# Kernel tuning notes

Measured on AMD Instinct MI355X. Metric: run time of the kernel, lower is better.

## Reference

```python
import jax, jax.numpy as jnp
import numpy as np
from jax import lax

B, Hm, Wm = 8, 128, 128          # batch, mesh height, mesh width
DIM, HEADS, DH, G, K = 128, 8, 64, 64, 3
INNER = HEADS * DH
N = Hm * Wm


def setup_inputs() -> dict:
    key = jax.random.key(0)
    ks = jax.random.split(key, 12)
    s = 0.02
    x = jax.random.normal(ks[0], (B, N, DIM), dtype=jnp.float32)
    conv_fx_w = jax.random.normal(ks[1], (K, K, DIM, INNER), dtype=jnp.float32) * s
    conv_fx_b = jnp.zeros((INNER,), dtype=jnp.float32)
    conv_x_w = jax.random.normal(ks[2], (K, K, DIM, INNER), dtype=jnp.float32) * s
    conv_x_b = jnp.zeros((INNER,), dtype=jnp.float32)
    # nn.Linear(dim_head, slice_num): weight (G, DH), orthogonal-init approximated by scaled normal
    slice_w = jax.random.normal(ks[3], (G, DH), dtype=jnp.float32) * (1.0 / np.sqrt(DH))
    slice_b = jnp.zeros((G,), dtype=jnp.float32)
    temperature = jnp.ones((1, HEADS, 1, 1), dtype=jnp.float32) * 0.5
    wq = jax.random.normal(ks[4], (DH, DH), dtype=jnp.float32) * s
    wk = jax.random.normal(ks[5], (DH, DH), dtype=jnp.float32) * s
    wv = jax.random.normal(ks[6], (DH, DH), dtype=jnp.float32) * s
    out_w = jax.random.normal(ks[7], (DIM, INNER), dtype=jnp.float32) * s
    out_b = jnp.zeros((DIM,), dtype=jnp.float32)
    return {
        "x": x,
        "conv_fx_w": conv_fx_w, "conv_fx_b": conv_fx_b,
        "conv_x_w": conv_x_w, "conv_x_b": conv_x_b,
        "slice_w": slice_w, "slice_b": slice_b,
        "temperature": temperature,
        "wq": wq, "wk": wk, "wv": wv,
        "out_w": out_w, "out_b": out_b,
    }


def _conv(z, w, b):
    # z: (B, H, W, Cin); w: (K, K, Cin, Cout); SAME padding, stride 1
    return lax.conv_general_dilated(
        z, w, window_strides=(1, 1), padding="SAME",
        dimension_numbers=("NHWC", "HWIO", "NHWC")) + b


def reference(x, conv_fx_w, conv_fx_b, conv_x_w, conv_x_b,
              slice_w, slice_b, temperature, wq, wk, wv, out_w, out_b):
    b, n, c = x.shape
    xi = x.reshape(b, Hm, Wm, c)
    # (B,H,W,INNER) -> (B,N,heads,dh) -> (B,heads,N,dh)
    fx_mid = _conv(xi, conv_fx_w, conv_fx_b).reshape(b, n, HEADS, DH).transpose(0, 2, 1, 3)
    x_mid = _conv(xi, conv_x_w, conv_x_b).reshape(b, n, HEADS, DH).transpose(0, 2, 1, 3)

    temp = jnp.clip(temperature, 0.1, 5.0)  # (1,heads,1,1)
    logits = (jnp.einsum("bhnc,gc->bhng", x_mid, slice_w) + slice_b) / temp
    slice_weights = jax.nn.softmax(logits, axis=-1)         # (B,heads,N,G)

    slice_norm = slice_weights.sum(axis=2)                   # (B,heads,G)
    slice_token = jnp.einsum("bhnc,bhng->bhgc", fx_mid, slice_weights)
    slice_token = slice_token / (slice_norm + 1e-5)[..., None]

    q = jnp.einsum("bhgc,dc->bhgd", slice_token, wq)
    k = jnp.einsum("bhgc,dc->bhgd", slice_token, wk)
    v = jnp.einsum("bhgc,dc->bhgd", slice_token, wv)

    scale = DH ** (-0.5)
    attn = jax.nn.softmax(jnp.einsum("bhgd,bhkd->bhgk", q, k) * scale, axis=-1)
    out_slice = jnp.einsum("bhgk,bhkd->bhgd", attn, v)       # (B,heads,G,dh)

    out_x = jnp.einsum("bhgc,bhng->bhnc", out_slice, slice_weights)
    out_x = out_x.transpose(0, 2, 1, 3).reshape(b, n, INNER)
    return jnp.einsum("bnc,dc->bnd", out_x, out_w) + out_b
```

## Files before the change

kernel.cpp:

```cpp
#include <hip/hip_runtime.h>
#include <stdint.h>

#define BATCH 8
#define HEADS 8
#define HM 128
#define WM 128
#define NPIX (HM*WM)
#define DIMC 128
#define DH 64
#define GS 64
#define INNER 512
#define KTOT 1152
#define XT_LD 128

typedef unsigned short u16;
typedef short v8s __attribute__((ext_vector_type(8)));
typedef float v4f __attribute__((ext_vector_type(4)));

__device__ __forceinline__ u16 f2bf(float f) {
    unsigned x = __float_as_uint(f);
    return (u16)((x + 0x7fffu + ((x >> 16) & 1u)) >> 16);
}
__device__ __forceinline__ float bf2f(u16 u) { return __uint_as_float(((unsigned)u) << 16); }
__device__ __forceinline__ unsigned cvtpk(float lo, float hi) {
    unsigned r;
    asm("v_cvt_pk_bf16_f32 %0, %1, %2" : "=v"(r) : "v"(lo), "v"(hi));
    return r;
}

union BF8 { uint4 v; u16 s[8]; };

__global__ __launch_bounds__(256) void k_build_w(
    const float* __restrict__ wx, const float* __restrict__ wfx,
    const float* __restrict__ slw, const float* __restrict__ temp,
    u16* __restrict__ wcatT, u16* __restrict__ wfxT)
{
    __shared__ float sw_l[GS][DH + 1];
    __shared__ float wx_l[INNER];
    int row = blockIdx.x;
    int t = threadIdx.x;
    for (int i = t; i < GS * DH; i += 256) sw_l[i >> 6][i & 63] = slw[i];
    for (int i = t; i < INNER; i += 256) wx_l[i] = wx[(size_t)row * INNER + i];
    __syncthreads();
#pragma unroll
    for (int j = 0; j < 2; j++) {
        int co = j * 256 + t;
        int h = co >> 6, g = co & 63;
        float s = 0.f;
        for (int c = 0; c < DH; c++) s = fmaf(wx_l[h * 64 + c], sw_l[g][c], s);
        float tv = fminf(fmaxf(temp[h], 0.1f), 5.0f);
        wcatT[(size_t)co * KTOT + row] = f2bf(s / tv);
        wfxT[(size_t)co * KTOT + row] = f2bf(wfx[(size_t)row * INNER + co]);
    }
}

__global__ __launch_bounds__(512) void k_build_b(
    const float* __restrict__ bx, const float* __restrict__ slw,
    const float* __restrict__ slb, const float* __restrict__ temp,
    float* __restrict__ bcatL)
{
    int co = threadIdx.x;
    int h = co >> 6, g = co & 63;
    float s = slb[g];
    for (int c = 0; c < DH; c++) s = fmaf(bx[h * 64 + c], slw[g * 64 + c], s);
    float tv = fminf(fmaxf(temp[h], 0.1f), 5.0f);
    bcatL[co] = s / tv;
}

union SmemC {
    u16 X[130 * XT_LD];
    struct { u16 SwT[64][128]; u16 FxT[64][128]; } e;
};

__global__ __launch_bounds__(256, 3) void k_conv2(
    const float* __restrict__ xin, const u16* __restrict__ wcatT,
    const u16* __restrict__ wfxT, const float* __restrict__ bcatL,
    const float* __restrict__ bfx, u16* __restrict__ swbT,
    float* __restrict__ straw, float* __restrict__ norm)
{
    __shared__ SmemC sm;
    int bid = blockIdx.x;
    int swz = (bid & 7) * 1024 + (bid >> 3);
    int b = swz >> 10;
    int r = swz & 1023;
    int y = r >> 3, h = r & 7;
    int cob = h << 6;
    int t = threadIdx.x;
    int lane = t & 63, wave = t >> 6;
    int half = wave >> 1, w_conv = wave & 1;
    int l16 = lane & 15, lk = lane >> 4;
    int bh = b * HEADS + h;

    v4f acc[4][4];
#pragma unroll
    for (int i = 0; i < 4; i++)
#pragma unroll
        for (int j = 0; j < 4; j++) acc[i][j] = v4f{0.f, 0.f, 0.f, 0.f};

    const u16* wT = w_conv ? wfxT : wcatT;
    const u16* wrb[4];
#pragma unroll
    for (int nj = 0; nj < 4; nj++)
        wrb[nj] = wT + (size_t)(cob + nj * 16 + l16) * KTOT + lk * 8;

    v8s bB[2][4];
#pragma unroll
    for (int nj = 0; nj < 4; nj++) bB[0][nj] = *(const v8s*)(wrb[nj]);

#pragma unroll
    for (int ky = 0; ky < 3; ky++) {
        int yy = y + ky - 1;
        bool yok = (unsigned)yy < (unsigned)HM;
        const float* xrow = xin + ((size_t)b * NPIX + (size_t)yy * WM) * DIMC;
        if (ky) __syncthreads();
#pragma unroll
        for (int it = 0; it < 9; it++) {
            int i = t + it * 256;
            if (i < 2080) {
                int row = i >> 4, k8 = i & 15;
                int px = row - 1;
                uint4 o;
                if (yok && (unsigned)px < (unsigned)WM) {
                    const float4* p = (const float4*)(xrow + (size_t)px * DIMC + k8 * 8);
                    float4 fa = p[0], fb = p[1];
                    o = make_uint4(cvtpk(fa.x, fa.y), cvtpk(fa.z, fa.w),
                                   cvtpk(fb.x, fb.y), cvtpk(fb.z, fb.w));
                } else {
                    o = make_uint4(0u, 0u, 0u, 0u);
                }
                *(uint4*)(sm.X + row * XT_LD + ((k8 ^ (row & 7)) * 8)) = o;
            }
        }
        __syncthreads();
#pragma unroll
        for (int cc = 0; cc < 12; cc++) {
            int gidx = ky * 12 + cc;
            if (gidx < 35) {
#pragma unroll
                for (int nj = 0; nj < 4; nj++)
                    bB[(gidx + 1) & 1][nj] = *(const v8s*)(wrb[nj] + (gidx + 1) * 32);
            }
            int kx = cc >> 2, c4 = cc & 3;
            int xr7 = (l16 + kx) & 7;
            const u16* xb = sm.X + (half * 64 + l16 + kx) * XT_LD;
            int xo = (((c4 * 4 + lk) ^ xr7) * 8);
            v8s av[4];
#pragma unroll
            for (int mi = 0; mi < 4; mi++)
                av[mi] = *(const v8s*)(xb + mi * 16 * XT_LD + xo);
#pragma unroll
            for (int mi = 0; mi < 4; mi++)
#pragma unroll
                for (int nj = 0; nj < 4; nj++)
                    acc[mi][nj] = __builtin_amdgcn_mfma_f32_16x16x32_bf16(
                        av[mi], bB[gidx & 1][nj], acc[mi][nj], 0, 0, 0);
        }
    }
    __syncthreads();

    float bb[4];
#pragma unroll
    for (int nj = 0; nj < 4; nj++)
        bb[nj] = (w_conv ? bfx : bcatL)[cob + nj * 16 + l16];

    if (w_conv == 0) {
#pragma unroll
        for (int mi = 0; mi < 4; mi++) {
#pragma unroll
            for (int q = 0; q < 4; q++) {
                float m = acc[mi][0][q] + bb[0];
#pragma unroll
                for (int nj = 1; nj < 4; nj++) m = fmaxf(m, acc[mi][nj][q] + bb[nj]);
                m = fmaxf(m, __shfl_xor(m, 1));
                m = fmaxf(m, __shfl_xor(m, 2));
                m = fmaxf(m, __shfl_xor(m, 4));
                m = fmaxf(m, __shfl_xor(m, 8));
                float ssum = 0.f;
#pragma unroll
                for (int nj = 0; nj < 4; nj++) {
                    float e = __expf(acc[mi][nj][q] + bb[nj] - m);
                    acc[mi][nj][q] = e; ssum += e;
                }
                ssum += __shfl_xor(ssum, 1);
                ssum += __shfl_xor(ssum, 2);
                ssum += __shfl_xor(ssum, 4);
                ssum += __shfl_xor(ssum, 8);
                float inv = 1.f / ssum;
#pragma unroll
                for (int nj = 0; nj < 4; nj++) acc[mi][nj][q] *= inv;
            }
        }
#pragma unroll
        for (int nj = 0; nj < 4; nj++) {
            float pn = 0.f;
#pragma unroll
            for (int mi = 0; mi < 4; mi++)
#pragma unroll
                for (int q = 0; q < 4; q++) pn += acc[mi][nj][q];
            pn += __shfl_xor(pn, 16);
            pn += __shfl_xor(pn, 32);
            if (lk == 0)
                atomicAdd(&norm[(size_t)bh * GS + nj * 16 + l16], pn);
        }
    }

#pragma unroll
    for (int nj = 0; nj < 4; nj++) {
        int grow = nj * 16 + l16;
        int r7 = l16 & 7;
#pragma unroll
        for (int mi = 0; mi < 4; mi++) {
            int p8 = half * 8 + mi * 2 + (lk >> 1);
            int off = ((p8 ^ r7) * 8) + (lk & 1) * 4;
            uint2 wv;
            if (w_conv == 0) {
                wv.x = cvtpk(acc[mi][nj][0], acc[mi][nj][1]);
                wv.y = cvtpk(acc[mi][nj][2], acc[mi][nj][3]);
                *(uint2*)&sm.e.SwT[grow][off] = wv;
            } else {
                wv.x = cvtpk(acc[mi][nj][0] + bb[nj], acc[mi][nj][1] + bb[nj]);
                wv.y = cvtpk(acc[mi][nj][2] + bb[nj], acc[mi][nj][3] + bb[nj]);
                *(uint2*)&sm.e.FxT[grow][off] = wv;
            }
        }
    }
    __syncthreads();

    {
        v4f pacc[4];
#pragma unroll
        for (int j = 0; j < 4; j++) pacc[j] = v4f{0.f, 0.f, 0.f, 0.f};
        int ga = wave * 16 + l16;
        int ra = ga & 7;
#pragma unroll
        for (int c = 0; c < 4; c++) {
            v8s aw = *(const v8s*)(&sm.e.SwT[ga][0] + (((c * 4 + lk) ^ ra) * 8));
            v8s bw[4];
#pragma unroll
            for (int nj = 0; nj < 4; nj++) {
                int dr = nj * 16 + l16;
                bw[nj] = *(const v8s*)(&sm.e.FxT[dr][0] + (((c * 4 + lk) ^ (dr & 7)) * 8));
            }
#pragma unroll
            for (int nj = 0; nj < 4; nj++)
                pacc[nj] = __builtin_amdgcn_mfma_f32_16x16x32_bf16(
                    aw, bw[nj], pacc[nj], 0, 0, 0);
        }
#pragma unroll
        for (int nj = 0; nj < 4; nj++)
#pragma unroll
            for (int q = 0; q < 4; q++) {
                int g = wave * 16 + lk * 4 + q;
                int dh = nj * 16 + l16;
                atomicAdd(&straw[((size_t)bh * GS + g) * DH + dh], pacc[nj][q]);
            }
    }

#pragma unroll
    for (int it = 0; it < 4; it++) {
        int chunk = it * 256 + t;
        int gi = chunk >> 4;
        int p8 = chunk & 15;
        uint4 v = *(const uint4*)(&sm.e.SwT[gi][0] + ((p8 ^ (gi & 7)) * 8));
        size_t di = (((size_t)bh * GS + gi) * NPIX) + (size_t)y * WM + p8 * 8;
        *(uint4*)&swbT[di] = v;
    }
}

__global__ __launch_bounds__(256) void k_attn(
    const float* __restrict__ straw, const float* __restrict__ norm,
    const float* __restrict__ wq, const float* __restrict__ wk, const float* __restrict__ wv,
    const float* __restrict__ outw, float* __restrict__ m1)
{
    __shared__ float lds[4][64][64];
    int bh = blockIdx.x, h = bh & 7;
    int t = threadIdx.x;
    for (int i = t; i < 4096; i += 256) {
        int g = i >> 6;
        lds[0][g][i & 63] = straw[(size_t)bh * 4096 + i] / (norm[bh * 64 + g] + 1e-5f);
    }
    __syncthreads();
    int g = t >> 2, d0 = (t & 3) << 4;
    for (int d = d0; d < d0 + 16; d++) {
        float sq = 0.f, sk = 0.f, sv = 0.f;
        for (int c = 0; c < 64; c++) {
            float sc = lds[0][g][c];
            sq = fmaf(sc, wq[d * 64 + c], sq);
            sk = fmaf(sc, wk[d * 64 + c], sk);
            sv = fmaf(sc, wv[d * 64 + c], sv);
        }
        lds[1][g][d] = sq; lds[2][g][d] = sk; lds[3][g][d] = sv;
    }
    __syncthreads();
    float attnrow[16];
    for (int k2 = d0, i = 0; k2 < d0 + 16; k2++, i++) {
        float s = 0.f;
        for (int d = 0; d < 64; d++) s = fmaf(lds[1][g][d], lds[2][k2][d], s);
        attnrow[i] = s * 0.125f;
    }
    __syncthreads();
    for (int i = 0; i < 16; i++) lds[0][g][d0 + i] = attnrow[i];
    __syncthreads();
    if (t < 64) {
        float mx = -1e30f;
        for (int j = 0; j < 64; j++) mx = fmaxf(mx, lds[0][t][j]);
        float s = 0.f;
        for (int j = 0; j < 64; j++) { float e = __expf(lds[0][t][j] - mx); lds[0][t][j] = e; s += e; }
        float inv = 1.f / s;
        for (int j = 0; j < 64; j++) lds[0][t][j] *= inv;
    }
    __syncthreads();
    float osrow[16];
    for (int d = d0, i = 0; d < d0 + 16; d++, i++) {
        float s = 0.f;
        for (int kx = 0; kx < 64; kx++) s = fmaf(lds[0][g][kx], lds[3][kx][d], s);
        osrow[i] = s;
    }
    __syncthreads();
    for (int i = 0; i < 16; i++) lds[2][g][d0 + i] = osrow[i];
    __syncthreads();
    int dimb = (t & 3) << 5;
    for (int dim = dimb; dim < dimb + 32; dim++) {
        float s = 0.f;
        for (int c = 0; c < 64; c++)
            s = fmaf(lds[2][g][c], outw[(size_t)dim * INNER + h * 64 + c], s);
        m1[((size_t)bh * 64 + g) * DIMC + dim] = s;
    }
}

__global__ __launch_bounds__(256) void k_final(
    const u16* __restrict__ swbT, const float* __restrict__ m1,
    const float* __restrict__ outb, float* __restrict__ out)
{
    __shared__ float As[32][68];
    __shared__ float Bs[32][128];
    int b = blockIdx.x, nt = blockIdx.y;
    int t = threadIdx.x;
    int tn = t & 15, tm = t >> 4;
    float acc[4][8];
#pragma unroll
    for (int i = 0; i < 4; i++)
#pragma unroll
        for (int j = 0; j < 8; j++) acc[i][j] = 0.f;
    int n0 = nt * 64;
    int gg = t >> 3, nq = (t & 7) * 8;
    int g2 = t >> 3, dd = (t & 7) * 16;
    for (int h = 0; h < HEADS; h++) {
        const u16* swp = swbT + (size_t)(b * HEADS + h) * GS * NPIX;
        const float* m1p = m1 + (size_t)(b * HEADS + h) * GS * DIMC;
        for (int g0 = 0; g0 < 64; g0 += 32) {
            __syncthreads();
            BF8 av8; av8.v = *(const uint4*)&swp[(size_t)(g0 + gg) * NPIX + n0 + nq];
#pragma unroll
            for (int i = 0; i < 8; i++) As[gg][nq + i] = bf2f(av8.s[i]);
            const float* bp = m1p + (size_t)(g0 + g2) * DIMC + dd;
            *(float4*)&Bs[g2][dd + 0]  = *(const float4*)(bp + 0);
            *(float4*)&Bs[g2][dd + 4]  = *(const float4*)(bp + 4);
            *(float4*)&Bs[g2][dd + 8]  = *(const float4*)(bp + 8);
            *(float4*)&Bs[g2][dd + 12] = *(const float4*)(bp + 12);
            __syncthreads();
#pragma unroll
            for (int kk = 0; kk < 32; kk++) {
                float4 a = *(const float4*)&As[kk][tm * 4];
                float4 b0 = *(const float4*)&Bs[kk][tn * 4];
                float4 b1 = *(const float4*)&Bs[kk][tn * 4 + 64];
                float av[4] = {a.x, a.y, a.z, a.w};
                float bv[8] = {b0.x, b0.y, b0.z, b0.w, b1.x, b1.y, b1.z, b1.w};
#pragma unroll
                for (int i = 0; i < 4; i++)
#pragma unroll
                    for (int j = 0; j < 8; j++)
                        acc[i][j] = fmaf(av[i], bv[j], acc[i][j]);
            }
        }
    }
    float4 bias0 = *(const float4*)&outb[tn * 4];
    float4 bias1 = *(const float4*)&outb[64 + tn * 4];
#pragma unroll
    for (int i = 0; i < 4; i++) {
        size_t n = (size_t)n0 + tm * 4 + i;
        size_t rb = ((size_t)b * NPIX + n) * DIMC;
        float4 r0, r1;
        r0.x = acc[i][0] + bias0.x; r0.y = acc[i][1] + bias0.y;
        r0.z = acc[i][2] + bias0.z; r0.w = acc[i][3] + bias0.w;
        r1.x = acc[i][4] + bias1.x; r1.y = acc[i][5] + bias1.y;
        r1.z = acc[i][6] + bias1.z; r1.w = acc[i][7] + bias1.w;
        *(float4*)&out[rb + tn * 4] = r0;
        *(float4*)&out[rb + 64 + tn * 4] = r1;
    }
}

extern "C" void kernel_launch(void* const* d_in, const int* in_sizes, int n_in,
                              void* d_out, int out_size, void* d_ws, size_t ws_size,
                              hipStream_t stream)
{
    (void)in_sizes; (void)n_in; (void)out_size;
    const float* x    = (const float*)d_in[0];
    const float* wfx  = (const float*)d_in[1];
    const float* bfx  = (const float*)d_in[2];
    const float* wx   = (const float*)d_in[3];
    const float* bx   = (const float*)d_in[4];
    const float* slw  = (const float*)d_in[5];
    const float* slb  = (const float*)d_in[6];
    const float* temp = (const float*)d_in[7];
    const float* wq   = (const float*)d_in[8];
    const float* wk   = (const float*)d_in[9];
    const float* wv   = (const float*)d_in[10];
    const float* outw = (const float*)d_in[11];
    const float* outb = (const float*)d_in[12];
    float* out = (float*)d_out;
    float* W = (float*)d_ws;

    u16*   wcatT = (u16*)W;
    u16*   wfxT  = (u16*)(W + 294912);
    float* bcatL = W + 589824;
    float* norm  = W + 590336;
    float* straw = W + 594432;
    float* m1    = W + 856576;
    u16*   swbT  = (u16*)(W + 1380864);
    const size_t need = 1380864ull * 4 + 67108864ull * 2;
    if (ws_size < need) return;

    hipMemsetAsync(norm, 0, (4096 + 262144) * sizeof(float), stream);

    k_build_w<<<dim3(1152), 256, 0, stream>>>(wx, wfx, slw, temp, wcatT, wfxT);
    k_build_b<<<dim3(1), 512, 0, stream>>>(bx, slw, slb, temp, bcatL);
    k_conv2<<<dim3(8192), 256, 0, stream>>>(x, wcatT, wfxT, bcatL, bfx, swbT, straw, norm);
    k_attn<<<dim3(64), 256, 0, stream>>>(straw, norm, wq, wk, wv, outw, m1);
    k_final<<<dim3(8, 256), 256, 0, stream>>>(swbT, m1, outb, out);
}
```

Baseline: 1.162 ms.

## Pre-convert input to swizzled bf16 and stage conv halo via direct global-to-LDS loads

Adds a pre-pass kernel that converts x to bf16 once, already XOR-swizzled per row, so the conv kernel no longer re-reads fp32 input and converts it for every head and row tile. The conv kernel then fills its halo tile with global_load_lds 16-byte loads, pointing padding slots at a small zero buffer. The LDS tile grows to 132 rows and the swizzle index is offset to match the new slot layout. The cost is an extra kernel launch and a bf16 copy of x in workspace, plus an explicit vmcnt wait before the barrier.

```diff
diff --git a/kernel.cpp b/kernel.cpp
--- a/kernel.cpp
+++ b/kernel.cpp
@@ -27,8 +27,27 @@
     asm("v_cvt_pk_bf16_f32 %0, %1, %2" : "=v"(r) : "v"(lo), "v"(hi));
     return r;
 }
+__device__ __forceinline__ void gload16(const u16* g, u16* ldst) {
+    __builtin_amdgcn_global_load_lds(
+        (const __attribute__((address_space(1))) void*)g,
+        (__attribute__((address_space(3))) void*)ldst, 16, 0, 0);
+}
 
 union BF8 { uint4 v; u16 s[8]; };
+
+__global__ __launch_bounds__(256) void k_xbf(
+    const float* __restrict__ x, u16* __restrict__ xbf)
+{
+    int i = blockIdx.x * 256 + threadIdx.x;
+    int rowg = i >> 4, k8 = i & 15;
+    const float* src = x + ((size_t)rowg * DIMC + k8 * 8);
+    float4 fa = *(const float4*)src;
+    float4 fb = *(const float4*)(src + 4);
+    uint4 o = make_uint4(cvtpk(fa.x, fa.y), cvtpk(fa.z, fa.w),
+                         cvtpk(fb.x, fb.y), cvtpk(fb.z, fb.w));
+    int s = k8 ^ (rowg & 7);
+    *(uint4*)(xbf + (size_t)rowg * DIMC + s * 8) = o;
+}
 
 __global__ __launch_bounds__(256) void k_build_w(
     const float* __restrict__ wx, const float* __restrict__ wfx,
@@ -68,15 +87,15 @@
 }
 
 union SmemC {
-    u16 X[130 * XT_LD];
+    u16 X[132 * XT_LD];
     struct { u16 SwT[64][128]; u16 FxT[64][128]; } e;
 };
 
 __global__ __launch_bounds__(256, 3) void k_conv2(
-    const float* __restrict__ xin, const u16* __restrict__ wcatT,
+    const u16* __restrict__ xbf, const u16* __restrict__ wcatT,
     const u16* __restrict__ wfxT, const float* __restrict__ bcatL,
-    const float* __restrict__ bfx, u16* __restrict__ swbT,
-    float* __restrict__ straw, float* __restrict__ norm)
+    const float* __restrict__ bfx, const u16* __restrict__ zbuf,
+    u16* __restrict__ swbT, float* __restrict__ straw, float* __restrict__ norm)
 {
     __shared__ SmemC sm;
     int bid = blockIdx.x;
@@ -111,26 +130,17 @@
     for (int ky = 0; ky < 3; ky++) {
         int yy = y + ky - 1;
         bool yok = (unsigned)yy < (unsigned)HM;
-        const float* xrow = xin + ((size_t)b * NPIX + (size_t)yy * WM) * DIMC;
+        const u16* xrowb = xbf + ((size_t)b * NPIX + (size_t)yy * WM) * DIMC;
         if (ky) __syncthreads();
-#pragma unroll
-        for (int it = 0; it < 9; it++) {
-            int i = t + it * 256;
-            if (i < 2080) {
-                int row = i >> 4, k8 = i & 15;
-                int px = row - 1;
-                uint4 o;
-                if (yok && (unsigned)px < (unsigned)WM) {
-                    const float4* p = (const float4*)(xrow + (size_t)px * DIMC + k8 * 8);
-                    float4 fa = p[0], fb = p[1];
-                    o = make_uint4(cvtpk(fa.x, fa.y), cvtpk(fa.z, fa.w),
-                                   cvtpk(fb.x, fb.y), cvtpk(fb.z, fb.w));
-                } else {
-                    o = make_uint4(0u, 0u, 0u, 0u);
-                }
-                *(uint4*)(sm.X + row * XT_LD + ((k8 ^ (row & 7)) * 8)) = o;
-            }
-        }
+        for (int j = wave; j < 33; j += 4) {
+            int slot = j * 64 + lane;
+            int row = slot >> 4, k8 = slot & 15;
+            int px = row - 1;
+            const u16* src = (yok && (unsigned)px < (unsigned)WM)
+                           ? xrowb + (size_t)px * DIMC + k8 * 8 : zbuf;
+            gload16(src, sm.X + j * 512);
+        }
+        asm volatile("s_waitcnt vmcnt(0)" ::: "memory");
         __syncthreads();
 #pragma unroll
         for (int cc = 0; cc < 12; cc++) {
@@ -141,7 +151,7 @@
                     bB[(gidx + 1) & 1][nj] = *(const v8s*)(wrb[nj] + (gidx + 1) * 32);
             }
             int kx = cc >> 2, c4 = cc & 3;
-            int xr7 = (l16 + kx) & 7;
+            int xr7 = (l16 + kx + 7) & 7;
             const u16* xb = sm.X + (half * 64 + l16 + kx) * XT_LD;
             int xo = (((c4 * 4 + lk) ^ xr7) * 8);
             v8s av[4];
@@ -414,18 +424,22 @@
     u16*   wcatT = (u16*)W;
     u16*   wfxT  = (u16*)(W + 294912);
     float* bcatL = W + 589824;
-    float* norm  = W + 590336;
-    float* straw = W + 594432;
-    float* m1    = W + 856576;
-    u16*   swbT  = (u16*)(W + 1380864);
-    const size_t need = 1380864ull * 4 + 67108864ull * 2;
+    float* zeros = W + 590336;
+    float* norm  = W + 590400;
+    float* straw = W + 594496;
+    float* m1    = W + 856640;
+    u16*   xbf   = (u16*)(W + 1380928);
+    u16*   swbT  = (u16*)(W + 9769536);
+    const size_t need = 9769536ull * 4 + 67108864ull * 2;
     if (ws_size < need) return;
 
-    hipMemsetAsync(norm, 0, (4096 + 262144) * sizeof(float), stream);
-
+    hipMemsetAsync(zeros, 0, (64 + 4096 + 262144) * sizeof(float), stream);
+
+    k_xbf<<<dim3(8192), 256, 0, stream>>>(x, xbf);
     k_build_w<<<dim3(1152), 256, 0, stream>>>(wx, wfx, slw, temp, wcatT, wfxT);
     k_build_b<<<dim3(1), 512, 0, stream>>>(bx, slw, slb, temp, bcatL);
-    k_conv2<<<dim3(8192), 256, 0, stream>>>(x, wcatT, wfxT, bcatL, bfx, swbT, straw, norm);
+    k_conv2<<<dim3(8192), 256, 0, stream>>>(xbf, wcatT, wfxT, bcatL, bfx,
+                                            (const u16*)zeros, swbT, straw, norm);
     k_attn<<<dim3(64), 256, 0, stream>>>(straw, norm, wq, wk, wv, outw, m1);
     k_final<<<dim3(8, 256), 256, 0, stream>>>(swbT, m1, outb, out);
 }
```

New measurement: 1.057 ms. -9.0%, faster.
